# Performance work log

Measured on AMD Instinct MI355X. Metric: run time of the kernel, lower is better.

The kernel has to match this reference:

```python
import jax, jax.numpy as jnp
import numpy as np

N = 20000   # nodes
E = 320000  # edges
H = 128     # hidden_dim
L = 4       # num_layers
OUT = 64    # output_dim
XD = 16     # node_input_dim


def setup_inputs() -> dict:
    key = jax.random.key(0)
    ks = jax.random.split(key, 32)

    def w(k, shape):
        fan_in = shape[-2] if len(shape) >= 2 else shape[-1]
        return (jax.random.normal(k, shape, jnp.float32) / np.sqrt(fan_in)).astype(jnp.float32)

    inp = {
        'y': jax.random.normal(ks[0], (N, 6), jnp.float32),
        'x': jax.random.normal(ks[1], (N, XD), jnp.float32),
        'edge_attr': jax.random.normal(ks[2], (E, 8), jnp.float32),
        'edge_index': jax.random.randint(ks[3], (2, E), 0, N),
        'W_node': w(ks[4], (XD, H)),        'b_node': jnp.zeros((H,), jnp.float32),
        'W_eemb': w(ks[5], (5, H - 3)),     'b_eemb': jnp.zeros((H - 3,), jnp.float32),
        'W_msg': w(ks[6], (L, 3 * H + 1, H)), 'b_msg': jnp.zeros((L, H), jnp.float32),
        'W_upd': w(ks[7], (L, 2 * H, H)),     'b_upd': jnp.zeros((L, H), jnp.float32),
        'ln_g': jnp.ones((L, H), jnp.float32), 'ln_b': jnp.zeros((L, H), jnp.float32),
        'W_eu': w(ks[8], (L, 3 * H, H)),      'b_eu': jnp.zeros((L, H), jnp.float32),
        'W_out': w(ks[9], (H, OUT)),          'b_out': jnp.zeros((OUT,), jnp.float32),
        'Wh1': w(ks[10], (OUT, OUT // 2)),    'bh1': jnp.zeros((OUT // 2,), jnp.float32),
        'Wh2': w(ks[11], (OUT // 2, 1)),      'bh2': jnp.zeros((1,), jnp.float32),
    }
    return inp


def _drift(y, x, edge_attr, W_node, b_node, W_eemb, b_eemb, W_msg, b_msg,
           W_upd, b_upd, ln_g, ln_b, W_eu, b_eu, W_out, b_out,
           Wh1, bh1, Wh2, bh2, edge_index):
    src, dst = edge_index[0], edge_index[1]
    q, p = jnp.split(y, 2, axis=-1)  # each [N,3]

    def potential(q):
        pos = q
        h = x @ W_node + b_node                                    # [N,H]
        e = jnp.concatenate([edge_attr[:, :3],
                             edge_attr[:, 3:] @ W_eemb + b_eemb], -1)  # [E,H]
        for l in range(L):
            rel = pos[dst] - pos[src]                              # [E,3]
            dist = jnp.sqrt(jnp.sum(rel * rel, -1, keepdims=True) + 1e-8)
            m_in = jnp.concatenate([h[src], h[dst], e, dist], -1)  # [E,3H+1]
            m = jax.nn.silu(m_in @ W_msg[l] + b_msg[l])            # [E,H]
            agg = jax.ops.segment_sum(m, dst, num_segments=N)      # [N,H]
            u = jnp.concatenate([h, agg], -1) @ W_upd[l] + b_upd[l]
            mu = jnp.mean(u, -1, keepdims=True)
            var = jnp.var(u, -1, keepdims=True)
            u = (u - mu) / jnp.sqrt(var + 1e-5) * ln_g[l] + ln_b[l]
            h = h + jax.nn.silu(u)
            e = e + jax.nn.silu(jnp.concatenate([h[src], h[dst], e], -1) @ W_eu[l] + b_eu[l])
        f = h @ W_out + b_out                                      # [N,OUT]
        v = jax.nn.silu(f @ Wh1 + bh1) @ Wh2 + bh2                 # [N,1]
        return jnp.sum(v)

    grad_q = jax.grad(potential)(q)      # dH/dq
    # dH/dp = p (kinetic 0.5*sum(p*p)); drift = (dH/dp, -dH/dq)
    return jnp.concatenate([p, -grad_q], axis=-1)


def reference(y, x, edge_attr, edge_index, W_node, b_node, W_eemb, b_eemb,
              W_msg, b_msg, W_upd, b_upd, ln_g, ln_b, W_eu, b_eu,
              W_out, b_out, Wh1, bh1, Wh2, bh2):
    return _drift(y, x, edge_attr, W_node, b_node, W_eemb, b_eemb, W_msg, b_msg,
                  W_upd, b_upd, ln_g, ln_b, W_eu, b_eu, W_out, b_out,
                  Wh1, bh1, Wh2, bh2, edge_index)
```

## Files before the change

kernel.cpp:

```cpp
#include <hip/hip_runtime.h>
#include <hip/hip_bf16.h>

#define NN 20000
#define NE 320000
#define H  128
#define NL 4

typedef unsigned int uint;
typedef unsigned short u16;
typedef short s8v __attribute__((ext_vector_type(8)));
typedef float fx4 __attribute__((ext_vector_type(4)));

static constexpr size_t NNH = (size_t)NN*H;
static constexpr size_t NEH = (size_t)NE*H;

static constexpr size_t OFF_H5    = 0;
static constexpr size_t OFF_UPRE  = OFF_H5    + 5*NNH*2;
static constexpr size_t OFF_LNST  = OFF_UPRE  + 4*NNH*2;
static constexpr size_t OFF_T     = OFF_LNST  + (size_t)4*NN*2*4;
static constexpr size_t OFF_E     = OFF_T     + 4*NNH*2;
static constexpr size_t OFF_DE    = OFF_E     + NEH*2;
static constexpr size_t OFF_AGG   = OFF_DE    + NEH*2;
static constexpr size_t OFF_DH    = OFF_AGG   + NNH*4;
static constexpr size_t OFF_DIST  = OFF_DH    + NNH*4;
static constexpr size_t OFF_DDIST = OFF_DIST  + (size_t)NE*4;
static constexpr size_t OFF_DPOS  = OFF_DDIST + (size_t)NE*4;
static constexpr size_t OFF_WMT   = OFF_DPOS  + (size_t)NN*3*4;
static constexpr size_t OFF_WET   = OFF_WMT   + (size_t)NL*128*388*4;
static constexpr size_t OFF_WUT   = OFF_WET   + (size_t)NL*128*384*4;
static constexpr size_t OFF_PD    = OFF_WUT   + (size_t)NL*128*256*4;
static constexpr size_t OFF_PS    = OFF_PD    + (size_t)NE*4;
static constexpr size_t OFF_CURD  = OFF_PS    + (size_t)NE*4;
static constexpr size_t OFF_CURS  = OFF_CURD  + (size_t)NN*4;
static constexpr size_t OFF_WMP   = OFF_CURS  + (size_t)NN*4;
static constexpr size_t OFF_WEP   = OFF_WMP   + (size_t)NL*49152*2;
static constexpr size_t OFF_WMTP  = OFF_WEP   + (size_t)NL*49152*2;
static constexpr size_t OFF_WETP  = OFF_WMTP  + (size_t)NL*49152*2;
static constexpr size_t WS_NEED   = OFF_WETP  + (size_t)NL*49152*2;

__device__ __forceinline__ float sigm(float x){ return 1.f/(1.f+__expf(-x)); }
__device__ __forceinline__ float siluf(float x){ return x*sigm(x); }
__device__ __forceinline__ float dsilu(float x){ float s=sigm(x); return s*(1.f + x*(1.f-s)); }
__device__ __forceinline__ u16 f2bf(float x){
  uint u = __float_as_uint(x);
  uint r = (u + 0x7fffu + ((u>>16)&1u)) >> 16;
  return (u16)r;
}
__device__ __forceinline__ float bf2f(u16 v){ return __uint_as_float(((uint)v)<<16); }
__device__ __forceinline__ uint pack2(float a, float b){ return (uint)f2bf(a) | ((uint)f2bf(b)<<16); }
__device__ __forceinline__ void ld_bf8(const u16* p, float* v){
  uint4 q = *(const uint4*)p;
  v[0]=__uint_as_float(q.x<<16); v[1]=__uint_as_float(q.x&0xffff0000u);
  v[2]=__uint_as_float(q.y<<16); v[3]=__uint_as_float(q.y&0xffff0000u);
  v[4]=__uint_as_float(q.z<<16); v[5]=__uint_as_float(q.z&0xffff0000u);
  v[6]=__uint_as_float(q.w<<16); v[7]=__uint_as_float(q.w&0xffff0000u);
}
__device__ __forceinline__ void st_bf8(u16* p, const float* v){
  uint4 o;
  o.x = pack2(v[0],v[1]); o.y = pack2(v[2],v[3]);
  o.z = pack2(v[4],v[5]); o.w = pack2(v[6],v[7]);
  *(uint4*)p = o;
}

__device__ __forceinline__ float2 blockSum2_128(float a, float b, float* sb){
  #pragma unroll
  for (int off=32; off>0; off>>=1){ a += __shfl_down(a, off); b += __shfl_down(b, off); }
  int t = threadIdx.x;
  if ((t&63)==0){ sb[(t>>6)*2+0]=a; sb[(t>>6)*2+1]=b; }
  __syncthreads();
  float2 r; r.x = sb[0]+sb[2]; r.y = sb[1]+sb[3];
  __syncthreads();
  return r;
}

__device__ __forceinline__ void seg_walk136(const u16* Cst, const int* keys, float* buf, int t){
  int c = t & 127, half = t >> 7;
  int i0 = half*64, i1 = i0 + 64;
  float acc = 0.f; int k = keys[i0];
  #pragma unroll 4
  for (int i=i0; i<i1; i++){
    int ki = keys[i];
    if (ki != k){ atomicAdd(&buf[(size_t)k*H + c], acc); acc = 0.f; k = ki; }
    acc += bf2f(Cst[(size_t)i*136 + c]);
  }
  atomicAdd(&buf[(size_t)k*H + c], acc);
}

__global__ void diag_k(float* out, float v){ out[0] = v; }

__global__ void hist_k(const int* __restrict__ ei, int* __restrict__ curs, int* __restrict__ curd){
  int e = blockIdx.x*256 + threadIdx.x;
  if (e >= NE) return;
  atomicAdd(&curs[ei[e]], 1);
  atomicAdd(&curd[ei[NE+e]], 1);
}

__global__ void scan_k(int* __restrict__ curd, int* __restrict__ curs){
  __shared__ int sm[256];
  for (int a=0; a<2; a++){
    int* p = a ? curs : curd;
    int run = 0;
    for (int base=0; base<NN; base+=256){
      int idx = base + threadIdx.x;
      sm[threadIdx.x] = (idx < NN) ? p[idx] : 0;
      __syncthreads();
      if (threadIdx.x == 0){
        int acc = run;
        for (int i=0;i<256;i++){ int v = sm[i]; sm[i] = acc; acc += v; }
        run = acc;
      }
      __syncthreads();
      if (idx < NN) p[idx] = sm[threadIdx.x];
      __syncthreads();
    }
  }
}

__global__ void fill_k(const int* __restrict__ ei, int* __restrict__ curs, int* __restrict__ curd,
                       int* __restrict__ perm_s, int* __restrict__ perm_d){
  int e = blockIdx.x*256 + threadIdx.x;
  if (e >= NE) return;
  perm_s[atomicAdd(&curs[ei[e]], 1)] = e;
  perm_d[atomicAdd(&curd[ei[NE+e]], 1)] = e;
}

__global__ void transpose_w(const float* __restrict__ Wm, const float* __restrict__ We,
                            const float* __restrict__ Wu,
                            float* __restrict__ WmT, float* __restrict__ WeT,
                            float* __restrict__ WuT){
  int idx = blockIdx.x*blockDim.x + threadIdx.x;
  int stride = gridDim.x*blockDim.x;
  for (int i=idx; i<NL*128*388; i+=stride){
    int l = i/(128*388), r = i - l*128*388, k = r/388, j = r - k*388;
    WmT[i] = (j<385) ? Wm[((size_t)l*385 + j)*H + k] : 0.f;
  }
  for (int i=idx; i<NL*128*384; i+=stride){
    int l = i/(128*384), r = i - l*128*384, k = r/384, j = r - k*384;
    WeT[i] = We[((size_t)l*384 + j)*H + k];
  }
  for (int i=idx; i<NL*128*256; i+=stride){
    int l = i/(128*256), r = i - l*128*256, k = r/256, j = r - k*256;
    WuT[i] = Wu[((size_t)l*256 + j)*H + k];
  }
}

__global__ __launch_bounds__(64) void pack_k(const float* __restrict__ src, u16* __restrict__ dst,
                      int KS, int NC, int ld, size_t sStride, size_t dStride){
  int b = blockIdx.x;
  int l = b/(KS*NC); int r = b - l*KS*NC; int ks = r/NC; int ct = r - ks*NC;
  int lane = threadIdx.x;
  #pragma unroll
  for (int j=0;j<8;j++){
    int k = ks*32 + (lane>>4)*8 + j;
    int c = ct*16 + (lane&15);
    dst[l*dStride + ((size_t)(ks*NC+ct)*64 + lane)*8 + j] =
        f2bf(src[l*sStride + (size_t)k*ld + c]);
  }
}

__global__ __launch_bounds__(128) void node_emb(const float* __restrict__ x,
                                                const float* __restrict__ Wn,
                                                const float* __restrict__ bn,
                                                u16* __restrict__ h){
  __shared__ float xs[16];
  int n = blockIdx.x, c = threadIdx.x;
  if (c < 16) xs[c] = x[(size_t)n*16 + c];
  __syncthreads();
  float s = bn[c];
  #pragma unroll
  for (int k=0;k<16;k++) s = fmaf(xs[k], Wn[k*H + c], s);
  h[(size_t)n*H + c] = f2bf(s);
}

__global__ __launch_bounds__(256) void edge_emb(const float* __restrict__ ea,
                                                const float* __restrict__ We5,
                                                const float* __restrict__ be,
                                                u16* __restrict__ ebuf){
  int e = blockIdx.x*2 + (threadIdx.x>>7);
  int c = threadIdx.x & 127;
  const float* row = ea + (size_t)e*8;
  float v;
  if (c < 3) v = row[c];
  else {
    int j = c-3;
    float s = be[j];
    #pragma unroll
    for (int k=0;k<5;k++) s = fmaf(row[3+k], We5[k*125 + j], s);
    v = s;
  }
  ebuf[(size_t)e*H + c] = f2bf(v);
}

__global__ void rel_dist(const float* __restrict__ y, const int* __restrict__ ei,
                         float* __restrict__ dist){
  int e = blockIdx.x*256 + threadIdx.x;
  if (e >= NE) return;
  int s = ei[e], d = ei[NE+e];
  float rx = y[(size_t)d*6+0] - y[(size_t)s*6+0];
  float ry = y[(size_t)d*6+1] - y[(size_t)s*6+1];
  float rz = y[(size_t)d*6+2] - y[(size_t)s*6+2];
  dist[e] = sqrtf(rx*rx + ry*ry + rz*rz + 1e-8f);
}

#define PHASE1_MFMA(ACC)                                                          \
  _Pragma("unroll 1")                                                             \
  for (int s=0; s<12; s++){                                                       \
    s8v av0, av1;                                                                 \
    {                                                                             \
      int k = s*32 + l4*8;                                                        \
      int row0 = wid*32 + li, row1 = row0 + 16;                                   \
      const u16 *p0, *p1;                                                         \
      if (k < 128){ p0 = hb + (size_t)sidx[row0]*H + k;                           \
                    p1 = hb + (size_t)sidx[row1]*H + k; }                         \
      else if (k < 256){ p0 = hb + (size_t)didx[row0]*H + (k-128);                \
                         p1 = hb + (size_t)didx[row1]*H + (k-128); }              \
      else { p0 = eb + (size_t)eidl[row0]*H + (k-256);                            \
             p1 = eb + (size_t)eidl[row1]*H + (k-256); }                          \
      av0 = *(const s8v*)p0; av1 = *(const s8v*)p1;                               \
    }                                                                             \
    _Pragma("unroll")                                                             \
    for (int ct=0; ct<8; ct++){                                                   \
      s8v bv = *(const s8v*)&WP[((size_t)(s*8+ct)*64 + lane)*8];                  \
      ACC[0][ct] = __builtin_amdgcn_mfma_f32_16x16x32_bf16(av0, bv, ACC[0][ct], 0,0,0); \
      ACC[1][ct] = __builtin_amdgcn_mfma_f32_16x16x32_bf16(av1, bv, ACC[1][ct], 0,0,0); \
    }                                                                             \
  }

template<int MODE>
__global__ __launch_bounds__(256) void efwd(
    const u16* __restrict__ hb, u16* __restrict__ eb,
    const float* __restrict__ dist, const int* __restrict__ ei,
    const int* __restrict__ perm,
    const float* __restrict__ Wf, const float* __restrict__ bias,
    const u16* __restrict__ WP,
    float* __restrict__ agg, float* __restrict__ Tf)
{
  __shared__ __align__(16) u16 Als[128*136];
  __shared__ int eidl[128], sidx[128], didx[128];
  const int t = threadIdx.x;
  const int e0 = blockIdx.x * 128;
  if (t < 128){
    int eid = perm ? perm[e0+t] : (e0+t);
    eidl[t] = eid; sidx[t] = ei[eid]; didx[t] = ei[NE+eid];
  }
  __syncthreads();
  const int lane = t&63, wid = t>>6, l4 = lane>>4, li = lane&15;

  fx4 acc[2][8];
  #pragma unroll
  for (int i=0;i<2;i++){
    #pragma unroll
    for (int j=0;j<8;j++) acc[i][j] = (fx4){0.f,0.f,0.f,0.f};
  }
  PHASE1_MFMA(acc)

  float dv[2][4];
  if (MODE==0){
    #pragma unroll
    for (int rt=0;rt<2;rt++){
      #pragma unroll
      for (int reg=0;reg<4;reg++) dv[rt][reg] = dist[eidl[wid*32+rt*16+l4*4+reg]];
    }
  }
  #pragma unroll
  for (int ct=0; ct<8; ct++){
    int c = ct*16 + li;
    float bi = bias[c];
    float wd = (MODE==0) ? Wf[(size_t)384*H + c] : 0.f;
    #pragma unroll
    for (int rt=0;rt<2;rt++){
      #pragma unroll
      for (int reg=0;reg<4;reg++)
        acc[rt][ct][reg] += bi + ((MODE==0) ? dv[rt][reg]*wd : 0.f);
    }
  }

  if (MODE==0){
    __syncthreads();
    #pragma unroll
    for (int rt=0;rt<2;rt++){
      #pragma unroll
      for (int reg=0;reg<4;reg++){
        int brow = wid*32+rt*16+l4*4+reg;
        #pragma unroll
        for (int ct=0;ct<8;ct++)
          Als[(size_t)brow*136 + ct*16+li] = f2bf(siluf(acc[rt][ct][reg]));
      }
    }
    __syncthreads();
    seg_walk136(Als, didx, agg, t);
    __syncthreads();
    #pragma unroll
    for (int rt=0;rt<2;rt++){
      #pragma unroll
      for (int reg=0;reg<4;reg++){
        int brow = wid*32+rt*16+l4*4+reg;
        #pragma unroll
        for (int ct=0;ct<8;ct++)
          Als[(size_t)brow*136 + ct*16+li] = f2bf(dsilu(acc[rt][ct][reg]));
      }
    }
    __syncthreads();
    seg_walk136(Als, didx, Tf, t);
  } else {
    __syncthreads();
    #pragma unroll
    for (int rt=0;rt<2;rt++){
      #pragma unroll
      for (int reg=0;reg<4;reg++){
        int brow = wid*32+rt*16+l4*4+reg;
        #pragma unroll
        for (int ct=0;ct<8;ct++)
          Als[(size_t)brow*136 + ct*16+li] = f2bf(siluf(acc[rt][ct][reg]));
      }
    }
    __syncthreads();
    int row = t>>1, coff = (t&1)*64;
    u16* dst = eb + (size_t)eidl[row]*H + coff;
    #pragma unroll
    for (int i=0;i<8;i++){
      float a[8], b[8];
      ld_bf8(&Als[(size_t)row*136 + coff + i*8], a);
      ld_bf8(&dst[i*8], b);
      #pragma unroll
      for (int j=0;j<8;j++) b[j] += a[j];
      st_bf8(&dst[i*8], b);
    }
  }
}

template<int MODE>
__global__ __launch_bounds__(256) void ebwd(
    const u16* __restrict__ hb, const u16* __restrict__ eb,
    const float* __restrict__ dist, const int* __restrict__ ei,
    const int* __restrict__ perm,
    const float* __restrict__ Wf, const float* __restrict__ bias,
    const float* __restrict__ mulf, const float* __restrict__ WTf,
    const u16* __restrict__ WP, const u16* __restrict__ WTP,
    float* __restrict__ dh, u16* __restrict__ de, float* __restrict__ ddist)
{
  __shared__ __align__(16) u16 Als[128*136];
  __shared__ int eidl[128], sidx[128], didx[128];
  const int t = threadIdx.x;
  const int e0 = blockIdx.x * 128;
  if (t < 128){
    int eid = perm[e0+t];
    eidl[t] = eid; sidx[t] = ei[eid]; didx[t] = ei[NE+eid];
  }
  __syncthreads();
  const int lane = t&63, wid = t>>6, l4 = lane>>4, li = lane&15;

  fx4 acc[2][8];
  #pragma unroll
  for (int i=0;i<2;i++){
    #pragma unroll
    for (int j=0;j<8;j++) acc[i][j] = (fx4){0.f,0.f,0.f,0.f};
  }
  PHASE1_MFMA(acc)

  float dv[2][4];
  if (MODE==0){
    #pragma unroll
    for (int rt=0;rt<2;rt++){
      #pragma unroll
      for (int reg=0;reg<4;reg++) dv[rt][reg] = dist[eidl[wid*32+rt*16+l4*4+reg]];
    }
  }
  #pragma unroll
  for (int ct=0; ct<8; ct++){
    int c = ct*16 + li;
    float bi = bias[c];
    float wd = (MODE==0) ? Wf[(size_t)384*H + c] : 0.f;
    #pragma unroll
    for (int rt=0;rt<2;rt++){
      #pragma unroll
      for (int reg=0;reg<4;reg++)
        acc[rt][ct][reg] += bi + ((MODE==0) ? dv[rt][reg]*wd : 0.f);
    }
  }

  if (MODE==1){
    {
      int row = t>>1, coff = (t&1)*64;
      const u16* src = de + (size_t)eidl[row]*H + coff;
      #pragma unroll
      for (int i=0;i<8;i++)
        *(uint4*)&Als[(size_t)row*136 + coff + i*8] = *(const uint4*)&src[i*8];
    }
    __syncthreads();
  }
  #pragma unroll
  for (int rt=0;rt<2;rt++){
    #pragma unroll
    for (int reg=0;reg<4;reg++){
      int brow = wid*32+rt*16+l4*4+reg;
      #pragma unroll
      for (int ct=0;ct<8;ct++){
        int c = ct*16+li;
        float m;
        if (MODE==0) m = mulf[(size_t)didx[brow]*H + c];
        else         m = bf2f(Als[(size_t)brow*136 + c]);
        acc[rt][ct][reg] = m * dsilu(acc[rt][ct][reg]);
      }
    }
  }

  if (MODE==0){
    float wdT[8];
    #pragma unroll
    for (int ct=0;ct<8;ct++) wdT[ct] = WTf[(size_t)(ct*16+li)*388 + 384];
    #pragma unroll
    for (int rt=0;rt<2;rt++){
      #pragma unroll
      for (int reg=0;reg<4;reg++){
        float pd = 0.f;
        #pragma unroll
        for (int ct=0;ct<8;ct++) pd = fmaf(acc[rt][ct][reg], wdT[ct], pd);
        pd += __shfl_xor(pd, 1);
        pd += __shfl_xor(pd, 2);
        pd += __shfl_xor(pd, 4);
        pd += __shfl_xor(pd, 8);
        if (li == 0) ddist[eidl[wid*32+rt*16+l4*4+reg]] += pd;
      }
    }
  }

  __syncthreads();
  #pragma unroll
  for (int rt=0;rt<2;rt++){
    #pragma unroll
    for (int reg=0;reg<4;reg++){
      int brow = wid*32+rt*16+l4*4+reg;
      #pragma unroll
      for (int ct=0;ct<8;ct++)
        Als[(size_t)brow*136 + ct*16+li] = f2bf(acc[rt][ct][reg]);
    }
  }
  __syncthreads();

  s8v afr[2][4];
  #pragma unroll
  for (int rt=0;rt<2;rt++){
    int row = wid*32 + rt*16 + li;
    #pragma unroll
    for (int ks=0;ks<4;ks++)
      afr[rt][ks] = *(const s8v*)&Als[(size_t)row*136 + ks*32 + l4*8];
  }

  const int njc = (MODE==0) ? 2 : 3;
  const int jcl[3] = {2, (MODE==0)?0:1, 0};
  #pragma unroll 1
  for (int ji=0; ji<njc; ji++){
    const int jc = jcl[ji];
    #pragma unroll
    for (int i=0;i<2;i++){
      #pragma unroll
      for (int j=0;j<8;j++) acc[i][j] = (fx4){0.f,0.f,0.f,0.f};
    }
    #pragma unroll
    for (int ks=0;ks<4;ks++){
      #pragma unroll
      for (int ct=0;ct<8;ct++){
        s8v bv = *(const s8v*)&WTP[((size_t)(ks*24 + jc*8 + ct)*64 + lane)*8];
        acc[0][ct] = __builtin_amdgcn_mfma_f32_16x16x32_bf16(afr[0][ks], bv, acc[0][ct], 0,0,0);
        acc[1][ct] = __builtin_amdgcn_mfma_f32_16x16x32_bf16(afr[1][ks], bv, acc[1][ct], 0,0,0);
      }
    }
    if (jc == 1){
      #pragma unroll
      for (int rt=0;rt<2;rt++){
        #pragma unroll
        for (int reg=0;reg<4;reg++){
          int dn = didx[wid*32+rt*16+l4*4+reg];
          #pragma unroll
          for (int ct=0;ct<8;ct++)
            atomicAdd(&dh[(size_t)dn*H + ct*16+li], acc[rt][ct][reg]);
        }
      }
    } else {
      __syncthreads();
      #pragma unroll
      for (int rt=0;rt<2;rt++){
        #pragma unroll
        for (int reg=0;reg<4;reg++){
          int brow = wid*32+rt*16+l4*4+reg;
          #pragma unroll
          for (int ct=0;ct<8;ct++)
            Als[(size_t)brow*136 + ct*16+li] = f2bf(acc[rt][ct][reg]);
        }
      }
      __syncthreads();
      if (jc == 2){
        int row = t>>1, coff = (t&1)*64;
        u16* dst = de + (size_t)eidl[row]*H + coff;
        #pragma unroll
        for (int i=0;i<8;i++){
          float a[8], b[8];
          ld_bf8(&Als[(size_t)row*136 + coff + i*8], a);
          ld_bf8(&dst[i*8], b);
          #pragma unroll
          for (int j=0;j<8;j++) b[j] += a[j];
          st_bf8(&dst[i*8], b);
        }
      } else {
        seg_walk136(Als, sidx, dh, t);
      }
    }
  }
}

__global__ __launch_bounds__(256) void tcvt_k(u16* __restrict__ T, float* __restrict__ Tf){
  size_t i = (size_t)blockIdx.x*256 + threadIdx.x;
  T[i] = f2bf(Tf[i]);
  Tf[i] = 0.f;
}

__global__ __launch_bounds__(128) void dstmsg_k(const float* __restrict__ dagg,
                                                const u16* __restrict__ T,
                                                const float* __restrict__ WmT,
                                                float* __restrict__ dh){
  __shared__ float s[128];
  int n = blockIdx.x, c = threadIdx.x;
  s[c] = dagg[(size_t)n*H + c] * bf2f(T[(size_t)n*H + c]);
  __syncthreads();
  float acc = 0.f;
  #pragma unroll 4
  for (int k=0;k<128;k++) acc = fmaf(s[k], WmT[(size_t)k*388 + 128 + c], acc);
  dh[(size_t)n*H + c] += acc;
}

__global__ __launch_bounds__(128) void upd_fwd(
    const u16* __restrict__ hin, const float* __restrict__ agg,
    const float* __restrict__ Wu, const float* __restrict__ bu,
    const float* __restrict__ g, const float* __restrict__ bln,
    u16* __restrict__ upre, float* __restrict__ lnst, u16* __restrict__ hout)
{
  __shared__ float ha[256];
  __shared__ float sb[4];
  int n = blockIdx.x, c = threadIdx.x;
  float hv = bf2f(hin[(size_t)n*H + c]);
  ha[c] = hv;
  ha[128+c] = agg[(size_t)n*H + c];
  __syncthreads();
  float s = bu[c];
  #pragma unroll 4
  for (int k=0;k<256;k++) s = fmaf(ha[k], Wu[(size_t)k*H + c], s);
  upre[(size_t)n*H + c] = f2bf(s);
  float2 ms = blockSum2_128(s, s*s, sb);
  float mu = ms.x*(1.f/128.f);
  float var = ms.y*(1.f/128.f) - mu*mu;
  float rstd = rsqrtf(var + 1e-5f);
  if (c == 0){ lnst[(size_t)n*2+0] = mu; lnst[(size_t)n*2+1] = rstd; }
  float uh = (s - mu)*rstd;
  float un = uh*g[c] + bln[c];
  hout[(size_t)n*H + c] = f2bf(hv + siluf(un));
}

__global__ __launch_bounds__(128) void final_fused(
    const u16* __restrict__ h, const float* __restrict__ Wo, const float* __restrict__ bo,
    const float* __restrict__ Wh1, const float* __restrict__ bh1v,
    const float* __restrict__ Wh2, float* __restrict__ dh)
{
  __shared__ float sh[128], sf[64], sdz[32], sdf[64];
  int n = blockIdx.x, c = threadIdx.x;
  sh[c] = bf2f(h[(size_t)n*H + c]);
  __syncthreads();
  if (c < 64){
    float s = bo[c];
    #pragma unroll 4
    for (int k=0;k<128;k++) s = fmaf(sh[k], Wo[(size_t)k*64 + c], s);
    sf[c] = s;
  }
  __syncthreads();
  if (c < 32){
    float s = bh1v[c];
    #pragma unroll 4
    for (int j=0;j<64;j++) s = fmaf(sf[j], Wh1[(size_t)j*32 + c], s);
    sdz[c] = Wh2[c]*dsilu(s);
  }
  __syncthreads();
  if (c < 64){
    float s = 0.f;
    #pragma unroll 4
    for (int k=0;k<32;k++) s = fmaf(sdz[k], Wh1[(size_t)c*32 + k], s);
    sdf[c] = s;
  }
  __syncthreads();
  {
    float s = 0.f;
    #pragma unroll 4
    for (int j=0;j<64;j++) s = fmaf(sdf[j], Wo[(size_t)c*64 + j], s);
    dh[(size_t)n*H + c] = s;
  }
}

__global__ __launch_bounds__(128) void upd_bwd(
    float* __restrict__ dh, float* __restrict__ dagg,
    const u16* __restrict__ upre, const float* __restrict__ lnst,
    const float* __restrict__ WuT,
    const float* __restrict__ g, const float* __restrict__ bln)
{
  __shared__ float sh[128];
  __shared__ float sb[4];
  int n = blockIdx.x, c = threadIdx.x;
  float up   = bf2f(upre[(size_t)n*H + c]);
  float mu   = lnst[(size_t)n*2+0];
  float rstd = lnst[(size_t)n*2+1];
  float uh = (up - mu)*rstd;
  float un = uh*g[c] + bln[c];
  float dhv = dh[(size_t)n*H + c];
  float dun = dhv * dsilu(un);
  float duh = dun * g[c];
  float2 m12 = blockSum2_128(duh, duh*uh, sb);
  float m1 = m12.x*(1.f/128.f), m2 = m12.y*(1.f/128.f);
  float dup = (duh - m1 - uh*m2)*rstd;
  sh[c] = dup;
  __syncthreads();
  float s0 = 0.f, s1 = 0.f;
  #pragma unroll 4
  for (int k=0;k<128;k++){
    float d = sh[k];
    s0 = fmaf(d, WuT[(size_t)k*256 + c], s0);
    s1 = fmaf(d, WuT[(size_t)k*256 + 128 + c], s1);
  }
  dh[(size_t)n*H + c] = dhv + s0;
  dagg[(size_t)n*H + c] = s1;
}

__global__ void rel_bwd(const float* __restrict__ y, const float* __restrict__ dist,
                        const float* __restrict__ ddist, const int* __restrict__ ei,
                        float* __restrict__ dpos){
  int e = blockIdx.x*256 + threadIdx.x;
  if (e >= NE) return;
  int s = ei[e], d = ei[NE+e];
  float gsc = ddist[e]/dist[e];
  #pragma unroll
  for (int i=0;i<3;i++){
    float dr = gsc*(y[(size_t)d*6+i] - y[(size_t)s*6+i]);
    atomicAdd(&dpos[(size_t)d*3+i],  dr);
    atomicAdd(&dpos[(size_t)s*3+i], -dr);
  }
}

__global__ void out_k(const float* __restrict__ y, const float* __restrict__ dpos,
                      float* __restrict__ out){
  int n = blockIdx.x*256 + threadIdx.x;
  if (n >= NN) return;
  #pragma unroll
  for (int i=0;i<3;i++) out[(size_t)n*6+i]   =  y[(size_t)n*6+3+i];
  #pragma unroll
  for (int i=0;i<3;i++) out[(size_t)n*6+3+i] = -dpos[(size_t)n*3+i];
}

extern "C" void kernel_launch(void* const* d_in, const int* in_sizes, int n_in,
                              void* d_out, int out_size, void* d_ws, size_t ws_size,
                              hipStream_t stream)
{
  const float* y   = (const float*)d_in[0];
  const float* x   = (const float*)d_in[1];
  const float* ea  = (const float*)d_in[2];
  const int*   ei  = (const int*)d_in[3];
  const float* Wn  = (const float*)d_in[4];
  const float* bn  = (const float*)d_in[5];
  const float* We5 = (const float*)d_in[6];
  const float* be5 = (const float*)d_in[7];
  const float* Wm  = (const float*)d_in[8];
  const float* bm  = (const float*)d_in[9];
  const float* Wu  = (const float*)d_in[10];
  const float* bu  = (const float*)d_in[11];
  const float* lg  = (const float*)d_in[12];
  const float* lb  = (const float*)d_in[13];
  const float* We  = (const float*)d_in[14];
  const float* beu = (const float*)d_in[15];
  const float* Wo  = (const float*)d_in[16];
  const float* bo  = (const float*)d_in[17];
  const float* Wh1 = (const float*)d_in[18];
  const float* bh1v= (const float*)d_in[19];
  const float* Wh2 = (const float*)d_in[20];
  float* out = (float*)d_out;

  if (ws_size < WS_NEED){
    diag_k<<<1, 1, 0, stream>>>(out, 4000.f + (float)(ws_size >> 20));
    return;
  }

  char* ws = (char*)d_ws;
  u16*   h5    = (u16*)  (ws + OFF_H5);
  u16*   upre  = (u16*)  (ws + OFF_UPRE);
  float* lnst  = (float*)(ws + OFF_LNST);
  u16*   T     = (u16*)  (ws + OFF_T);
  u16*   eb    = (u16*)  (ws + OFF_E);
  u16*   de    = (u16*)  (ws + OFF_DE);
  float* aggd  = (float*)(ws + OFF_AGG);
  float* dh    = (float*)(ws + OFF_DH);
  float* dist  = (float*)(ws + OFF_DIST);
  float* ddist = (float*)(ws + OFF_DDIST);
  float* dpos  = (float*)(ws + OFF_DPOS);
  float* WmT   = (float*)(ws + OFF_WMT);
  float* WeT   = (float*)(ws + OFF_WET);
  float* WuT   = (float*)(ws + OFF_WUT);
  int*   perm_d= (int*)  (ws + OFF_PD);
  int*   perm_s= (int*)  (ws + OFF_PS);
  int*   curd  = (int*)  (ws + OFF_CURD);
  int*   curs  = (int*)  (ws + OFF_CURS);
  u16*   WmP   = (u16*)  (ws + OFF_WMP);
  u16*   WeP   = (u16*)  (ws + OFF_WEP);
  u16*   WmTP  = (u16*)  (ws + OFF_WMTP);
  u16*   WeTP  = (u16*)  (ws + OFF_WETP);

  hipMemsetAsync(ddist, 0, (size_t)NE*4, stream);
  hipMemsetAsync(dpos,  0, (size_t)NN*3*4, stream);
  hipMemsetAsync(de,    0, NEH*2, stream);
  hipMemsetAsync(dh,    0, NNH*4, stream);
  hipMemsetAsync(curd,  0, (size_t)NN*4, stream);
  hipMemsetAsync(curs,  0, (size_t)NN*4, stream);

  transpose_w<<<512, 256, 0, stream>>>(Wm, We, Wu, WmT, WeT, WuT);
  pack_k<<<NL*12*8, 64, 0, stream>>>(Wm,  WmP,  12, 8,  128, (size_t)385*128, 49152);
  pack_k<<<NL*12*8, 64, 0, stream>>>(We,  WeP,  12, 8,  128, (size_t)384*128, 49152);
  pack_k<<<NL*4*24, 64, 0, stream>>>(WmT, WmTP, 4,  24, 388, (size_t)128*388, 49152);
  pack_k<<<NL*4*24, 64, 0, stream>>>(WeT, WeTP, 4,  24, 384, (size_t)128*384, 49152);

  node_emb<<<NN, 128, 0, stream>>>(x, Wn, bn, h5);
  edge_emb<<<NE/2, 256, 0, stream>>>(ea, We5, be5, eb);
  rel_dist<<<NE/256, 256, 0, stream>>>(y, ei, dist);

  hist_k<<<NE/256, 256, 0, stream>>>(ei, curs, curd);
  scan_k<<<1, 256, 0, stream>>>(curd, curs);
  fill_k<<<NE/256, 256, 0, stream>>>(ei, curs, curd, perm_s, perm_d);

  for (int l=0; l<NL; l++){
    hipMemsetAsync(aggd, 0, NNH*4, stream);
    efwd<0><<<NE/128, 256, 0, stream>>>(h5 + l*NNH, eb, dist, ei, perm_d,
        Wm + (size_t)l*385*H, bm + (size_t)l*H, WmP + (size_t)l*49152, aggd, dh);
    tcvt_k<<<(int)(NNH/256), 256, 0, stream>>>(T + l*NNH, dh);
    upd_fwd<<<NN, 128, 0, stream>>>(h5 + l*NNH, aggd,
        Wu + (size_t)l*256*H, bu + (size_t)l*H,
        lg + (size_t)l*H, lb + (size_t)l*H,
        upre + l*NNH, lnst + (size_t)l*NN*2, h5 + (l+1)*NNH);
    if (l < NL-1){
      efwd<1><<<NE/128, 256, 0, stream>>>(h5 + (l+1)*NNH, eb, nullptr, ei, nullptr,
          We + (size_t)l*384*H, beu + (size_t)l*H, WeP + (size_t)l*49152, nullptr, nullptr);
    }
  }

  final_fused<<<NN, 128, 0, stream>>>(h5 + (size_t)NL*NNH, Wo, bo, Wh1, bh1v, Wh2, dh);

  for (int l=NL-1; l>=0; l--){
    if (l < NL-1){
      edge_emb<<<NE/2, 256, 0, stream>>>(ea, We5, be5, eb);
      for (int k=0; k<l; k++){
        efwd<1><<<NE/128, 256, 0, stream>>>(h5 + (k+1)*NNH, eb, nullptr, ei, nullptr,
            We + (size_t)k*384*H, beu + (size_t)k*H, WeP + (size_t)k*49152, nullptr, nullptr);
      }
      ebwd<1><<<NE/128, 256, 0, stream>>>(h5 + (l+1)*NNH, eb, nullptr, ei, perm_s,
          We + (size_t)l*384*H, beu + (size_t)l*H, nullptr, nullptr,
          WeP + (size_t)l*49152, WeTP + (size_t)l*49152, dh, de, nullptr);
    }
    upd_bwd<<<NN, 128, 0, stream>>>(dh, aggd, upre + l*NNH, lnst + (size_t)l*NN*2,
        WuT + (size_t)l*128*256, lg + (size_t)l*H, lb + (size_t)l*H);
    dstmsg_k<<<NN, 128, 0, stream>>>(aggd, T + l*NNH, WmT + (size_t)l*128*388, dh);
    ebwd<0><<<NE/128, 256, 0, stream>>>(h5 + l*NNH, eb, dist, ei, perm_s,
        Wm + (size_t)l*385*H, bm + (size_t)l*H, aggd, WmT + (size_t)l*128*388,
        WmP + (size_t)l*49152, WmTP + (size_t)l*49152, dh, de, ddist);
  }

  rel_bwd<<<NE/256, 256, 0, stream>>>(y, dist, ddist, ei, dpos);
  out_k<<<(NN+255)/256, 256, 0, stream>>>(y, dpos, out);
}
```

Measured before the change: 4.556 ms.

## Batch 8 nodes per block in node kernels, fuse tcvt and dstmsg, parallelize scan

Node-level kernels (upd_fwd, final_fused, upd_bwd) now process 8 nodes per block, so each weight value loaded from global memory is reused across 8 nodes instead of one. The tcvt conversion is folded into upd_fwd and the dstmsg matmul into upd_bwd, which removes two kernel launches and their extra passes over node arrays. The single-thread serial scan is replaced by per-thread chunk sums plus a Hillis-Steele prefix in shared memory. In exchange each block holds more shared memory and registers, there are fewer blocks, and the LayerNorm reductions across the 8 nodes run one after another.

```diff
diff --git a/kernel.cpp b/kernel.cpp
--- a/kernel.cpp
+++ b/kernel.cpp
@@ -95,24 +95,27 @@
   atomicAdd(&curd[ei[NE+e]], 1);
 }
 
-__global__ void scan_k(int* __restrict__ curd, int* __restrict__ curs){
-  __shared__ int sm[256];
+__global__ __launch_bounds__(256) void scan_k(int* __restrict__ curd, int* __restrict__ curs){
+  __shared__ int ps[256];
+  const int t = threadIdx.x;
+  const int CH = (NN + 255)/256;
   for (int a=0; a<2; a++){
     int* p = a ? curs : curd;
-    int run = 0;
-    for (int base=0; base<NN; base+=256){
-      int idx = base + threadIdx.x;
-      sm[threadIdx.x] = (idx < NN) ? p[idx] : 0;
+    int lo = t*CH, hi = lo+CH < NN ? lo+CH : NN;
+    int sum = 0;
+    for (int i=lo; i<hi; i++) sum += p[i];
+    ps[t] = sum;
+    __syncthreads();
+    #pragma unroll
+    for (int off=1; off<256; off<<=1){
+      int v = (t>=off) ? ps[t-off] : 0;
       __syncthreads();
-      if (threadIdx.x == 0){
-        int acc = run;
-        for (int i=0;i<256;i++){ int v = sm[i]; sm[i] = acc; acc += v; }
-        run = acc;
-      }
+      ps[t] += v;
       __syncthreads();
-      if (idx < NN) p[idx] = sm[threadIdx.x];
-      __syncthreads();
-    }
+    }
+    int run = (t==0) ? 0 : ps[t-1];
+    for (int i=lo; i<hi; i++){ int v = p[i]; p[i] = run; run += v; }
+    __syncthreads();
   }
 }
 
@@ -509,51 +512,49 @@
   }
 }
 
-__global__ __launch_bounds__(256) void tcvt_k(u16* __restrict__ T, float* __restrict__ Tf){
-  size_t i = (size_t)blockIdx.x*256 + threadIdx.x;
-  T[i] = f2bf(Tf[i]);
-  Tf[i] = 0.f;
-}
-
-__global__ __launch_bounds__(128) void dstmsg_k(const float* __restrict__ dagg,
-                                                const u16* __restrict__ T,
-                                                const float* __restrict__ WmT,
-                                                float* __restrict__ dh){
-  __shared__ float s[128];
-  int n = blockIdx.x, c = threadIdx.x;
-  s[c] = dagg[(size_t)n*H + c] * bf2f(T[(size_t)n*H + c]);
-  __syncthreads();
-  float acc = 0.f;
-  #pragma unroll 4
-  for (int k=0;k<128;k++) acc = fmaf(s[k], WmT[(size_t)k*388 + 128 + c], acc);
-  dh[(size_t)n*H + c] += acc;
-}
-
 __global__ __launch_bounds__(128) void upd_fwd(
     const u16* __restrict__ hin, const float* __restrict__ agg,
     const float* __restrict__ Wu, const float* __restrict__ bu,
     const float* __restrict__ g, const float* __restrict__ bln,
-    u16* __restrict__ upre, float* __restrict__ lnst, u16* __restrict__ hout)
+    u16* __restrict__ upre, float* __restrict__ lnst, u16* __restrict__ hout,
+    u16* __restrict__ T, float* __restrict__ Tf)
 {
-  __shared__ float ha[256];
+  __shared__ float ha[8][256];
   __shared__ float sb[4];
-  int n = blockIdx.x, c = threadIdx.x;
-  float hv = bf2f(hin[(size_t)n*H + c]);
-  ha[c] = hv;
-  ha[128+c] = agg[(size_t)n*H + c];
-  __syncthreads();
-  float s = bu[c];
-  #pragma unroll 4
-  for (int k=0;k<256;k++) s = fmaf(ha[k], Wu[(size_t)k*H + c], s);
-  upre[(size_t)n*H + c] = f2bf(s);
-  float2 ms = blockSum2_128(s, s*s, sb);
-  float mu = ms.x*(1.f/128.f);
-  float var = ms.y*(1.f/128.f) - mu*mu;
-  float rstd = rsqrtf(var + 1e-5f);
-  if (c == 0){ lnst[(size_t)n*2+0] = mu; lnst[(size_t)n*2+1] = rstd; }
-  float uh = (s - mu)*rstd;
-  float un = uh*g[c] + bln[c];
-  hout[(size_t)n*H + c] = f2bf(hv + siluf(un));
+  const int n0 = blockIdx.x*8, c = threadIdx.x;
+  #pragma unroll
+  for (int n=0;n<8;n++){
+    ha[n][c]     = bf2f(hin[(size_t)(n0+n)*H + c]);
+    ha[n][128+c] = agg[(size_t)(n0+n)*H + c];
+  }
+  __syncthreads();
+  float s[8];
+  float bv = bu[c];
+  #pragma unroll
+  for (int n=0;n<8;n++) s[n] = bv;
+  #pragma unroll 2
+  for (int k=0;k<256;k++){
+    float w = Wu[(size_t)k*H + c];
+    #pragma unroll
+    for (int n=0;n<8;n++) s[n] = fmaf(ha[n][k], w, s[n]);
+  }
+  float gc = g[c], bc = bln[c];
+  #pragma unroll 1
+  for (int n=0;n<8;n++){
+    int nn = n0+n;
+    upre[(size_t)nn*H + c] = f2bf(s[n]);
+    float2 ms = blockSum2_128(s[n], s[n]*s[n], sb);
+    float mu = ms.x*(1.f/128.f);
+    float var = ms.y*(1.f/128.f) - mu*mu;
+    float rstd = rsqrtf(var + 1e-5f);
+    if (c == 0){ lnst[(size_t)nn*2+0] = mu; lnst[(size_t)nn*2+1] = rstd; }
+    float uh = (s[n] - mu)*rstd;
+    float un = uh*gc + bc;
+    hout[(size_t)nn*H + c] = f2bf(ha[n][c] + siluf(un));
+    size_t idx = (size_t)nn*H + c;
+    T[idx] = f2bf(Tf[idx]);
+    Tf[idx] = 0.f;
+  }
 }
 
 __global__ __launch_bounds__(128) void final_fused(
@@ -561,70 +562,129 @@
     const float* __restrict__ Wh1, const float* __restrict__ bh1v,
     const float* __restrict__ Wh2, float* __restrict__ dh)
 {
-  __shared__ float sh[128], sf[64], sdz[32], sdf[64];
-  int n = blockIdx.x, c = threadIdx.x;
-  sh[c] = bf2f(h[(size_t)n*H + c]);
+  __shared__ float sh[8][128], sf[8][64], sdz[8][32], sdf[8][64];
+  const int n0 = blockIdx.x*8, c = threadIdx.x;
+  #pragma unroll
+  for (int n=0;n<8;n++) sh[n][c] = bf2f(h[(size_t)(n0+n)*H + c]);
   __syncthreads();
   if (c < 64){
-    float s = bo[c];
-    #pragma unroll 4
-    for (int k=0;k<128;k++) s = fmaf(sh[k], Wo[(size_t)k*64 + c], s);
-    sf[c] = s;
+    float s[8]; float bv = bo[c];
+    #pragma unroll
+    for (int n=0;n<8;n++) s[n] = bv;
+    #pragma unroll 2
+    for (int k=0;k<128;k++){
+      float w = Wo[(size_t)k*64 + c];
+      #pragma unroll
+      for (int n=0;n<8;n++) s[n] = fmaf(sh[n][k], w, s[n]);
+    }
+    #pragma unroll
+    for (int n=0;n<8;n++) sf[n][c] = s[n];
   }
   __syncthreads();
   if (c < 32){
-    float s = bh1v[c];
-    #pragma unroll 4
-    for (int j=0;j<64;j++) s = fmaf(sf[j], Wh1[(size_t)j*32 + c], s);
-    sdz[c] = Wh2[c]*dsilu(s);
+    float s[8]; float bv = bh1v[c];
+    #pragma unroll
+    for (int n=0;n<8;n++) s[n] = bv;
+    #pragma unroll 2
+    for (int j=0;j<64;j++){
+      float w = Wh1[(size_t)j*32 + c];
+      #pragma unroll
+      for (int n=0;n<8;n++) s[n] = fmaf(sf[n][j], w, s[n]);
+    }
+    float w2 = Wh2[c];
+    #pragma unroll
+    for (int n=0;n<8;n++) sdz[n][c] = w2*dsilu(s[n]);
   }
   __syncthreads();
   if (c < 64){
-    float s = 0.f;
-    #pragma unroll 4
-    for (int k=0;k<32;k++) s = fmaf(sdz[k], Wh1[(size_t)c*32 + k], s);
-    sdf[c] = s;
+    float s[8];
+    #pragma unroll
+    for (int n=0;n<8;n++) s[n] = 0.f;
+    #pragma unroll 2
+    for (int k=0;k<32;k++){
+      float w = Wh1[(size_t)c*32 + k];
+      #pragma unroll
+      for (int n=0;n<8;n++) s[n] = fmaf(sdz[n][k], w, s[n]);
+    }
+    #pragma unroll
+    for (int n=0;n<8;n++) sdf[n][c] = s[n];
   }
   __syncthreads();
   {
-    float s = 0.f;
-    #pragma unroll 4
-    for (int j=0;j<64;j++) s = fmaf(sdf[j], Wo[(size_t)c*64 + j], s);
-    dh[(size_t)n*H + c] = s;
+    float s[8];
+    #pragma unroll
+    for (int n=0;n<8;n++) s[n] = 0.f;
+    #pragma unroll 2
+    for (int j=0;j<64;j++){
+      float w = Wo[(size_t)c*64 + j];
+      #pragma unroll
+      for (int n=0;n<8;n++) s[n] = fmaf(sdf[n][j], w, s[n]);
+    }
+    #pragma unroll
+    for (int n=0;n<8;n++) dh[(size_t)(n0+n)*H + c] = s[n];
   }
 }
 
 __global__ __launch_bounds__(128) void upd_bwd(
     float* __restrict__ dh, float* __restrict__ dagg,
     const u16* __restrict__ upre, const float* __restrict__ lnst,
-    const float* __restrict__ WuT,
+    const float* __restrict__ WuT, const u16* __restrict__ T,
+    const float* __restrict__ WmT,
     const float* __restrict__ g, const float* __restrict__ bln)
 {
-  __shared__ float sh[128];
+  __shared__ float sh[8][128];
+  __shared__ float qs[8][128];
   __shared__ float sb[4];
-  int n = blockIdx.x, c = threadIdx.x;
-  float up   = bf2f(upre[(size_t)n*H + c]);
-  float mu   = lnst[(size_t)n*2+0];
-  float rstd = lnst[(size_t)n*2+1];
-  float uh = (up - mu)*rstd;
-  float un = uh*g[c] + bln[c];
-  float dhv = dh[(size_t)n*H + c];
-  float dun = dhv * dsilu(un);
-  float duh = dun * g[c];
-  float2 m12 = blockSum2_128(duh, duh*uh, sb);
-  float m1 = m12.x*(1.f/128.f), m2 = m12.y*(1.f/128.f);
-  float dup = (duh - m1 - uh*m2)*rstd;
-  sh[c] = dup;
-  __syncthreads();
-  float s0 = 0.f, s1 = 0.f;
-  #pragma unroll 4
+  const int n0 = blockIdx.x*8, c = threadIdx.x;
+  const float gc = g[c], bc = bln[c];
+  float dhv[8];
+  #pragma unroll 1
+  for (int n=0;n<8;n++){
+    int nn = n0+n;
+    float up   = bf2f(upre[(size_t)nn*H + c]);
+    float mu   = lnst[(size_t)nn*2+0];
+    float rstd = lnst[(size_t)nn*2+1];
+    float uh = (up - mu)*rstd;
+    float un = uh*gc + bc;
+    dhv[n] = dh[(size_t)nn*H + c];
+    float dun = dhv[n] * dsilu(un);
+    float duh = dun * gc;
+    float2 m12 = blockSum2_128(duh, duh*uh, sb);
+    sh[n][c] = (duh - m12.x*(1.f/128.f) - uh*(m12.y*(1.f/128.f)))*rstd;
+  }
+  __syncthreads();
+  float s0[8], s1[8];
+  #pragma unroll
+  for (int n=0;n<8;n++){ s0[n]=0.f; s1[n]=0.f; }
+  #pragma unroll 2
   for (int k=0;k<128;k++){
-    float d = sh[k];
-    s0 = fmaf(d, WuT[(size_t)k*256 + c], s0);
-    s1 = fmaf(d, WuT[(size_t)k*256 + 128 + c], s1);
-  }
-  dh[(size_t)n*H + c] = dhv + s0;
-  dagg[(size_t)n*H + c] = s1;
+    float w0 = WuT[(size_t)k*256 + c];
+    float w1 = WuT[(size_t)k*256 + 128 + c];
+    #pragma unroll
+    for (int n=0;n<8;n++){
+      float d = sh[n][k];
+      s0[n] = fmaf(d, w0, s0[n]);
+      s1[n] = fmaf(d, w1, s1[n]);
+    }
+  }
+  #pragma unroll
+  for (int n=0;n<8;n++){
+    int nn = n0+n;
+    dagg[(size_t)nn*H + c] = s1[n];
+    qs[n][c] = s1[n] * bf2f(T[(size_t)nn*H + c]);
+  }
+  __syncthreads();
+  float a2[8];
+  #pragma unroll
+  for (int n=0;n<8;n++) a2[n] = 0.f;
+  #pragma unroll 2
+  for (int k=0;k<128;k++){
+    float w = WmT[(size_t)k*388 + 128 + c];
+    #pragma unroll
+    for (int n=0;n<8;n++) a2[n] = fmaf(qs[n][k], w, a2[n]);
+  }
+  #pragma unroll
+  for (int n=0;n<8;n++) dh[(size_t)(n0+n)*H + c] = dhv[n] + s0[n] + a2[n];
 }
 
 __global__ void rel_bwd(const float* __restrict__ y, const float* __restrict__ dist,
@@ -733,18 +793,18 @@
     hipMemsetAsync(aggd, 0, NNH*4, stream);
     efwd<0><<<NE/128, 256, 0, stream>>>(h5 + l*NNH, eb, dist, ei, perm_d,
         Wm + (size_t)l*385*H, bm + (size_t)l*H, WmP + (size_t)l*49152, aggd, dh);
-    tcvt_k<<<(int)(NNH/256), 256, 0, stream>>>(T + l*NNH, dh);
-    upd_fwd<<<NN, 128, 0, stream>>>(h5 + l*NNH, aggd,
+    upd_fwd<<<NN/8, 128, 0, stream>>>(h5 + l*NNH, aggd,
         Wu + (size_t)l*256*H, bu + (size_t)l*H,
         lg + (size_t)l*H, lb + (size_t)l*H,
-        upre + l*NNH, lnst + (size_t)l*NN*2, h5 + (l+1)*NNH);
+        upre + l*NNH, lnst + (size_t)l*NN*2, h5 + (l+1)*NNH,
+        T + l*NNH, dh);
     if (l < NL-1){
       efwd<1><<<NE/128, 256, 0, stream>>>(h5 + (l+1)*NNH, eb, nullptr, ei, nullptr,
           We + (size_t)l*384*H, beu + (size_t)l*H, WeP + (size_t)l*49152, nullptr, nullptr);
     }
   }
 
-  final_fused<<<NN, 128, 0, stream>>>(h5 + (size_t)NL*NNH, Wo, bo, Wh1, bh1v, Wh2, dh);
+  final_fused<<<NN/8, 128, 0, stream>>>(h5 + (size_t)NL*NNH, Wo, bo, Wh1, bh1v, Wh2, dh);
 
   for (int l=NL-1; l>=0; l--){
     if (l < NL-1){
@@ -757,9 +817,9 @@
           We + (size_t)l*384*H, beu + (size_t)l*H, nullptr, nullptr,
           WeP + (size_t)l*49152, WeTP + (size_t)l*49152, dh, de, nullptr);
     }
-    upd_bwd<<<NN, 128, 0, stream>>>(dh, aggd, upre + l*NNH, lnst + (size_t)l*NN*2,
-        WuT + (size_t)l*128*256, lg + (size_t)l*H, lb + (size_t)l*H);
-    dstmsg_k<<<NN, 128, 0, stream>>>(aggd, T + l*NNH, WmT + (size_t)l*128*388, dh);
+    upd_bwd<<<NN/8, 128, 0, stream>>>(dh, aggd, upre + l*NNH, lnst + (size_t)l*NN*2,
+        WuT + (size_t)l*128*256, T + l*NNH, WmT + (size_t)l*128*388,
+        lg + (size_t)l*H, lb + (size_t)l*H);
     ebwd<0><<<NE/128, 256, 0, stream>>>(h5 + l*NNH, eb, dist, ei, perm_s,
         Wm + (size_t)l*385*H, bm + (size_t)l*H, aggd, WmT + (size_t)l*128*388,
         WmP + (size_t)l*49152, WmTP + (size_t)l*49152, dh, de, ddist);
```

Result: faster. 3.780 ms (-17.0%).
